# Performance work log

Measured on AMD Instinct MI355X. Metric: run time of the kernel, lower is better.

The kernel has to match this reference:

```python
import jax, jax.numpy as jnp
import numpy as np

# Dimensions (see shape_source)
U, B, D, H = 1024, 8, 512, 8
CHUNK = 32
NC = U // CHUNK          # 32 chunks
R, S, M = 32, 32, 32     # right-context rows, summary, memory
K = 31                   # depthwise conv kernel
Q = R + U + S            # 1088
KV = M + R + U           # 1088
NEG_INF = -1.0e8


def _build_attention_mask():
    """Chunk-wise Emformer mask: True = disallowed connection.
    Q layout: [R right-context rows | U utterance rows | S summary rows].
    KV layout: [M memory cols | R right-context cols | U utterance cols].
    Chunk c attends: memory banks < c, its own right-context col,
    its own chunk plus 1 left-context chunk of utterance."""
    mask = np.ones((Q, KV), dtype=bool)
    for c in range(NC):
        cols = np.zeros(KV, dtype=bool)
        cols[:min(c, M)] = True                    # memory of prior chunks
        cols[M + c] = True                         # this chunk's right context
        lo = max(0, c - 1) * CHUNK                 # 1 chunk of left context
        hi = (c + 1) * CHUNK
        cols[M + R + lo:M + R + hi] = True
        rows = [c] + list(range(R + c * CHUNK, R + (c + 1) * CHUNK)) + [R + U + c]
        mask[np.ix_(rows, np.nonzero(cols)[0])] = False
    return mask


def setup_inputs() -> dict:
    key = jax.random.key(0)
    ks = jax.random.split(key, 16)
    s = D ** -0.5
    inp = {
        'utterance': jax.random.normal(ks[0], (U, B, D), jnp.float32),
        'right_context': jax.random.normal(ks[1], (R, B, D), jnp.float32),
        'summary': jax.random.normal(ks[2], (S, B, D), jnp.float32),
        'memory': jax.random.normal(ks[3], (M, B, D), jnp.float32),
        'w_q': jax.random.normal(ks[4], (D, D), jnp.float32) * s,
        'b_q': jnp.zeros((D,), jnp.float32),
        'w_kv': jax.random.normal(ks[5], (2 * D, D), jnp.float32) * s,
        'b_kv': jnp.zeros((2 * D,), jnp.float32),
        'w_out': jax.random.normal(ks[6], (D, D), jnp.float32) * s,
        'b_out': jnp.zeros((D,), jnp.float32),
        'w_pw1': jax.random.normal(ks[7], (2 * D, D), jnp.float32) * s,
        'b_pw1': jnp.zeros((2 * D,), jnp.float32),
        'w_dw': jax.random.normal(ks[8], (D, 1, K), jnp.float32) * (K ** -0.5),
        'b_dw': jnp.zeros((D,), jnp.float32),
        'ln_g': jnp.ones((D,), jnp.float32),
        'ln_b': jnp.zeros((D,), jnp.float32),
        'w_pw2': jax.random.normal(ks[9], (D, D), jnp.float32) * s,
        'b_pw2': jnp.zeros((D,), jnp.float32),
        'lengths': jax.random.randint(ks[10], (B,), U // 2, U + 1, jnp.int32),
        'attention_mask': jnp.asarray(_build_attention_mask()),
    }
    return inp


def _conv_module(x, w_pw1, b_pw1, w_dw, b_dw, ln_g, ln_b, w_pw2, b_pw2):
    # x: (T, B, C) -> (B, C, T)
    x = x.transpose(1, 2, 0)
    x = jnp.einsum('bct,oc->bot', x, w_pw1) + b_pw1[:, None]
    a, g = jnp.split(x, 2, axis=1)
    x = a * jax.nn.sigmoid(g)                       # GLU over channel dim
    pad = (K - 1) // 2
    x = jax.lax.conv_general_dilated(
        x, w_dw, (1,), [(pad, pad)],
        dimension_numbers=('NCH', 'OIH', 'NCH'),
        feature_group_count=x.shape[1]) + b_dw[:, None]
    x = x.transpose(0, 2, 1)                        # (B, T, C) for LayerNorm
    mu = x.mean(-1, keepdims=True)
    var = ((x - mu) ** 2).mean(-1, keepdims=True)
    x = (x - mu) * jax.lax.rsqrt(var + 1e-5) * ln_g + ln_b
    x = x.transpose(0, 2, 1)
    x = x * jax.nn.sigmoid(x)                       # Swish
    x = jnp.einsum('bct,oc->bot', x, w_pw2) + b_pw2[:, None]
    return x.transpose(2, 0, 1)                     # (T, B, C)


def _emformer_forward(utterance, right_context, summary, memory,
                      w_q, b_q, w_kv, b_kv, w_out, b_out,
                      w_pw1, b_pw1, w_dw, b_dw, ln_g, ln_b, w_pw2, b_pw2,
                      lengths, attention_mask):
    d = D // H
    scaling = d ** -0.5
    q_in = jnp.concatenate([right_context, utterance, summary], axis=0)   # (Q,B,D)
    query = q_in @ w_q.T + b_q
    kv_in = jnp.concatenate([memory, right_context, utterance], axis=0)   # (KV,B,D)
    kv = kv_in @ w_kv.T + b_kv
    key_t, value_t = jnp.split(kv, 2, axis=2)

    def heads(t):  # (T,B,D) -> (B*H, T, d)
        return t.reshape(t.shape[0], B * H, d).transpose(1, 0, 2)

    qh, kh, vh = heads(query) * scaling, heads(key_t), heads(value_t)
    w = jnp.einsum('bqd,bkd->bqk', qh, kh)                                # (B*H,Q,KV)
    w = jnp.where(attention_mask[None], NEG_INF, w)
    # padding mask: pad positions are kv index >= KV - U + length
    pad = jnp.arange(KV)[None, :] >= (KV - U + lengths)[:, None]          # (B,KV)
    w = jnp.where(pad[:, None, :].repeat(H, axis=1).reshape(B * H, 1, KV), NEG_INF, w)
    p = jax.nn.softmax(w, axis=-1)
    attn = jnp.einsum('bqk,bkd->bqd', p, vh)                              # (B*H,Q,d)
    attn = attn.transpose(1, 0, 2).reshape(Q, B, D)
    outputs = attn @ w_out.T + b_out
    out_ru = outputs[:R + U]                                              # (R+U,B,D)
    # conformer convolution module with residual
    conv_out = _conv_module(out_ru, w_pw1, b_pw1, w_dw, b_dw,
                            ln_g, ln_b, w_pw2, b_pw2)
    return out_ru + conv_out


def reference(utterance, right_context, summary, memory,
              w_q, b_q, w_kv, b_kv, w_out, b_out,
              w_pw1, b_pw1, w_dw, b_dw, ln_g, ln_b, w_pw2, b_pw2,
              lengths, attention_mask):
    return _emformer_forward(utterance, right_context, summary, memory,
                             w_q, b_q, w_kv, b_kv, w_out, b_out,
                             w_pw1, b_pw1, w_dw, b_dw, ln_g, ln_b,
                             w_pw2, b_pw2, lengths, attention_mask)
```

## Files before the change

kernel.cpp:

```cpp
#include <hip/hip_runtime.h>
#include <hip/hip_bf16.h>
#include <math.h>

#define TQ    1056
#define TKV   1088

typedef __attribute__((ext_vector_type(8))) short short8;
typedef __attribute__((ext_vector_type(4))) short short4v;
typedef __attribute__((ext_vector_type(4))) float float4v;
typedef unsigned short ushort_t;

__device__ inline ushort_t f2bf(float x){
  union{float f; unsigned u;} v; v.f = x;
  unsigned r = v.u + 0x7fff + ((v.u >> 16) & 1);
  return (ushort_t)(r >> 16);
}
__device__ inline float bf2f(ushort_t h){
  union{unsigned u; float f;} v; v.u = ((unsigned)h) << 16;
  return v.f;
}

__device__ inline void gl_lds16(const ushort_t* g, ushort_t* l){
  __builtin_amdgcn_global_load_lds(
      (const __attribute__((address_space(1))) unsigned int*)g,
      (__attribute__((address_space(3))) unsigned int*)l, 16, 0, 0);
}

struct Cvt9 {
  const float* s[8];
  ushort_t*    d[8];
  const float* wdw;
  float*       wdwT;
  int bstart[9];
};

__global__ __launch_bounds__(256)
void cvt_f32_bf16(Cvt9 a)
{
  int blk = blockIdx.x;
  if (blk >= a.bstart[8]){
    int k = blk - a.bstart[8];
    int c = threadIdx.x;
    a.wdwT[k * 512 + c]       = a.wdw[c * 31 + k];
    a.wdwT[k * 512 + c + 256] = a.wdw[(c + 256) * 31 + k];
    return;
  }
  int seg = 0;
  while (blk >= a.bstart[seg + 1]) ++seg;
  int local = blk - a.bstart[seg];
  int idx = (local * 256 + threadIdx.x) * 4;
  float4v v = *(const float4v*)(a.s[seg] + idx);
  short4v o;
  #pragma unroll
  for (int j = 0; j < 4; ++j) ((ushort_t*)&o)[j] = f2bf(v[j]);
  *(short4v*)(a.d[seg] + idx) = o;
}

template<int MODE, int NX, int NT>
__global__ __launch_bounds__(256)
void gemm_bf16(const ushort_t* __restrict__ A, const ushort_t* __restrict__ Wb,
               const float* __restrict__ bias, const float* __restrict__ bias2,
               const ushort_t* __restrict__ residb,
               float* __restrict__ C0, ushort_t* __restrict__ U0,
               ushort_t* __restrict__ U1, ushort_t* __restrict__ Uv, int ny)
{
  constexpr int JN = NT / 32;
  const int blk = blockIdx.x;
  const int xcd = blk & 7;
  const int j   = blk >> 3;
  const int n_idx = j % NX;
  const int m_idx = (j / NX) * 8 + xcd;
  if (m_idx >= ny) return;

  __shared__ __align__(16) ushort_t As[128 * 64];
  __shared__ __align__(16) ushort_t Bs[NT * 64];
  const int tid  = threadIdx.x;
  const int w    = tid >> 6;
  const int lane = tid & 63;
  const int quad = lane >> 4;
  const int l16  = lane & 15;
  const int n0 = n_idx * NT;
  const int m0 = m_idx * 128;
  const int wm = (w >> 1) * 64;
  const int wn = (w & 1) * (NT / 2);
  const int srow = tid >> 3;
  const int skseg = tid & 7;

  float4v acc[4][JN];
  #pragma unroll
  for (int i = 0; i < 4; ++i)
    #pragma unroll
    for (int jj = 0; jj < JN; ++jj)
      acc[i][jj] = (float4v)(0.f);

  for (int kt = 0; kt < 8; ++kt){
    const int k0 = kt * 64;
    #pragma unroll
    for (int s = 0; s < 4; ++s){
      int row = s*32 + srow;
      gl_lds16(A + (size_t)(m0 + row) * 512 + k0 + ((skseg ^ (row & 7)) << 3),
               &As[row * 64 + (skseg << 3)]);
    }
    #pragma unroll
    for (int s = 0; s < NT/32; ++s){
      int row = s*32 + srow;
      gl_lds16(Wb + (size_t)(n0 + row) * 512 + k0 + ((skseg ^ (row & 7)) << 3),
               &Bs[row * 64 + (skseg << 3)]);
    }
    __syncthreads();
    #pragma unroll
    for (int kc = 0; kc < 2; ++kc){
      const int col = (((quad + (kc << 2)) ^ (l16 & 7)) << 3);
      short8 af[4], bf[JN];
      #pragma unroll
      for (int i = 0; i < 4; ++i)
        af[i] = *(const short8*)&As[(wm + i*16 + l16) * 64 + col];
      #pragma unroll
      for (int jj = 0; jj < JN; ++jj)
        bf[jj] = *(const short8*)&Bs[(wn + jj*16 + l16) * 64 + col];
      #pragma unroll
      for (int i = 0; i < 4; ++i)
        #pragma unroll
        for (int jj = 0; jj < JN; ++jj)
          acc[i][jj] = __builtin_amdgcn_mfma_f32_16x16x32_bf16(
                          af[i], bf[jj], acc[i][jj], 0, 0, 0);
    }
    __syncthreads();
  }

  #pragma unroll
  for (int jj = 0; jj < JN; ++jj){
    const int n = n0 + wn + jj*16 + l16;
    const float bn = (MODE == 4) ? (n < 512 ? bias[n] : bias2[(n - 512) & 1023])
                                 : bias[n];
    #pragma unroll
    for (int i = 0; i < 4; ++i){
      #pragma unroll
      for (int reg = 0; reg < 4; ++reg){
        const int m = m0 + wm + i*16 + quad*4 + reg;
        float v = acc[i][jj][reg] + bn;
        if (MODE == 4){
          int t = m >> 3, b = m & 7;
          if (n < 512){
            if (m >= 256){
              int mq = m - 256;
              int tq = mq >> 3, bq = mq & 7;
              int h = n >> 6, dh = n & 63;
              U0[(((size_t)(bq*8 + h)) * TQ + tq) * 64 + dh] = f2bf(v * 0.125f);
            }
          } else {
            int n2 = n & 511;
            int h = n2 >> 6, dh = n2 & 63;
            ushort_t* dst = (n < 1024) ? U1 : Uv;
            dst[(((size_t)(b*8 + h)) * TKV + t) * 64 + dh] = f2bf(v);
          }
        } else if (MODE == 0){
          U0[(size_t)m * 512 + n] = f2bf(v);
        } else {
          v += bf2f(residb[(size_t)m * 512 + n]);
          C0[(size_t)m * 512 + n] = v;
        }
      }
    }
  }
}

__global__ __launch_bounds__(256)
void transpose_v(const ushort_t* __restrict__ vh, ushort_t* __restrict__ vt)
{
  const int t0 = blockIdx.x * 64;
  const int bh = blockIdx.y;
  const int tid = threadIdx.x;
  __shared__ __align__(16) ushort_t T[64 * 72];

  #pragma unroll
  for (int e = 0; e < 2; ++e){
    int idx = e * 256 + tid;
    int r = idx >> 3, sg = (idx & 7) * 8;
    *(short8*)&T[r * 72 + sg] =
        *(const short8*)&vh[(((size_t)bh) * TKV + t0 + r) * 64 + sg];
  }
  __syncthreads();

  const int dh = tid & 63;
  const int ts = (tid >> 6) * 16;
  short8 v0, v1;
  #pragma unroll
  for (int j = 0; j < 8; ++j){
    ((ushort_t*)&v0)[j] = T[(ts + j) * 72 + dh];
    ((ushort_t*)&v1)[j] = T[(ts + 8 + j) * 72 + dh];
  }
  const size_t ob = (((size_t)bh) * 64 + dh) * TKV + t0 + ts;
  *(short8*)&vt[ob]     = v0;
  *(short8*)&vt[ob + 8] = v1;
}

#define PSTR 136

__global__ __launch_bounds__(256)
void attn_mfma(const ushort_t* __restrict__ qh, const ushort_t* __restrict__ kh,
               const ushort_t* __restrict__ vt, const int* __restrict__ lengths,
               ushort_t* __restrict__ attn_out)
{
  const int c  = blockIdx.x;
  const int bh = blockIdx.y;
  const int b  = bh >> 3, h = bh & 7;
  const int tid = threadIdx.x;
  const int w   = tid >> 6;
  const int lane = tid & 63;
  const int quad = lane >> 4;
  const int l16  = lane & 15;
  const int len  = lengths[b];
  const int tb2 = 64 + (c > 0 ? c - 1 : 0) * 32;
  const int tb3 = 64 + c * 32;

  __shared__ __align__(16) ushort_t Ps[48 * PSTR];

  const int basew = (w == 0) ? 0 : (w == 1) ? 32 : (w == 2) ? tb2 : tb3;

  float4v Sf[3][2];
  #pragma unroll
  for (int mt = 0; mt < 3; ++mt)
    #pragma unroll
    for (int jt = 0; jt < 2; ++jt)
      Sf[mt][jt] = (float4v)(0.f);

  #pragma unroll
  for (int kc = 0; kc < 2; ++kc){
    short8 bfr[2];
    #pragma unroll
    for (int jt = 0; jt < 2; ++jt)
      bfr[jt] = *(const short8*)&kh[((size_t)bh * TKV + basew + jt*16 + l16) * 64
                                    + kc*32 + quad*8];
    #pragma unroll
    for (int mt = 0; mt < 3; ++mt){
      int trow = (mt == 0) ? c : 32 + c*32 + (mt-1)*16 + l16;
      short8 afr = *(const short8*)&qh[((size_t)bh * TQ + trow) * 64
                                       + kc*32 + quad*8];
      if (mt == 0 && l16 != 0){
        short8 z = {0,0,0,0,0,0,0,0};
        afr = z;
      }
      #pragma unroll
      for (int jt = 0; jt < 2; ++jt)
        Sf[mt][jt] = __builtin_amdgcn_mfma_f32_16x16x32_bf16(
                        afr, bfr[jt], Sf[mt][jt], 0, 0, 0);
    }
  }

  bool live[2];
  #pragma unroll
  for (int jt = 0; jt < 2; ++jt){
    int jcol = jt*16 + l16;
    if      (w == 0) live[jt] = (jcol < c);
    else if (w == 1) live[jt] = (jcol == c);
    else if (w == 2) live[jt] = (c > 0) && ((c-1)*32 + jcol < len);
    else             live[jt] = (c*32 + jcol < len);
  }
  #pragma unroll
  for (int mt = 0; mt < 3; ++mt)
    #pragma unroll
    for (int jt = 0; jt < 2; ++jt)
      #pragma unroll
      for (int r = 0; r < 4; ++r){
        int row = mt*16 + quad*4 + r;
        Ps[row * PSTR + w*32 + jt*16 + l16] =
            live[jt] ? f2bf(__expf(Sf[mt][jt][r])) : (ushort_t)0;
      }
  __syncthreads();

  const short8 ones = {0x3F80,0x3F80,0x3F80,0x3F80,0x3F80,0x3F80,0x3F80,0x3F80};
  float4v Of[3], Ls[3];
  #pragma unroll
  for (int mt = 0; mt < 3; ++mt){ Of[mt] = (float4v)(0.f); Ls[mt] = (float4v)(0.f); }
  #pragma unroll
  for (int kc = 0; kc < 4; ++kc){
    const int tbase = (kc == 0) ? 0 : (kc == 1) ? 32 : (kc == 2) ? tb2 : tb3;
    short8 bv = *(const short8*)&vt[((size_t)bh * 64 + w*16 + l16) * TKV
                                    + tbase + quad*8];
    #pragma unroll
    for (int mt = 0; mt < 3; ++mt){
      short8 ap = *(const short8*)&Ps[(mt*16 + l16) * PSTR + kc*32 + quad*8];
      Of[mt] = __builtin_amdgcn_mfma_f32_16x16x32_bf16(ap, bv,   Of[mt], 0,0,0);
      Ls[mt] = __builtin_amdgcn_mfma_f32_16x16x32_bf16(ap, ones, Ls[mt], 0,0,0);
    }
  }

  #pragma unroll
  for (int mt = 0; mt < 3; ++mt){
    #pragma unroll
    for (int r = 0; r < 4; ++r){
      int row = mt*16 + quad*4 + r;
      if (mt == 0 && row != 0) continue;
      float o = Of[mt][r] / Ls[mt][r];
      int t = (mt == 0) ? c : 32 + c*32 + (row - 16);
      attn_out[(((size_t)t) * 8 + b) * 512 + h*64 + w*16 + l16] = f2bf(o);
    }
  }
}

__global__ __launch_bounds__(256)
void gemm_pw1_glu(const ushort_t* __restrict__ A, const ushort_t* __restrict__ Wb,
                  const float* __restrict__ bias, ushort_t* __restrict__ G, int ny)
{
  const int blk = blockIdx.x;
  const int xcd = blk & 7;
  const int j   = blk >> 3;
  const int n_idx = j % 8;
  const int m_idx = (j / 8) * 8 + xcd;
  if (m_idx >= ny) return;

  __shared__ __align__(16) ushort_t As [128 * 64];
  __shared__ __align__(16) ushort_t Bsa[64 * 64];
  __shared__ __align__(16) ushort_t Bsg[64 * 64];
  const int tid  = threadIdx.x;
  const int w    = tid >> 6;
  const int lane = tid & 63;
  const int quad = lane >> 4;
  const int l16  = lane & 15;
  const int n0 = n_idx * 64;
  const int m0 = m_idx * 128;
  const int wm = (w >> 1) * 64;
  const int wn = (w & 1) * 32;
  const int srow = tid >> 3;
  const int skseg = tid & 7;

  float4v acca[4][2], accg[4][2];
  #pragma unroll
  for (int i = 0; i < 4; ++i)
    #pragma unroll
    for (int jj = 0; jj < 2; ++jj){
      acca[i][jj] = (float4v)(0.f);
      accg[i][jj] = (float4v)(0.f);
    }

  for (int kt = 0; kt < 8; ++kt){
    const int k0 = kt * 64;
    #pragma unroll
    for (int s = 0; s < 4; ++s){
      int row = s*32 + srow;
      gl_lds16(A + (size_t)(m0 + row) * 512 + k0 + ((skseg ^ (row & 7)) << 3),
               &As[row * 64 + (skseg << 3)]);
    }
    #pragma unroll
    for (int s = 0; s < 2; ++s){
      int row = s*32 + srow;
      gl_lds16(Wb + (size_t)(n0 + row) * 512 + k0 + ((skseg ^ (row & 7)) << 3),
               &Bsa[row * 64 + (skseg << 3)]);
      gl_lds16(Wb + (size_t)(n0 + 512 + row) * 512 + k0 + ((skseg ^ (row & 7)) << 3),
               &Bsg[row * 64 + (skseg << 3)]);
    }
    __syncthreads();
    #pragma unroll
    for (int kc = 0; kc < 2; ++kc){
      const int col = (((quad + (kc << 2)) ^ (l16 & 7)) << 3);
      short8 af[4], ba[2], bg[2];
      #pragma unroll
      for (int i = 0; i < 4; ++i)
        af[i] = *(const short8*)&As[(wm + i*16 + l16) * 64 + col];
      #pragma unroll
      for (int jj = 0; jj < 2; ++jj){
        ba[jj] = *(const short8*)&Bsa[(wn + jj*16 + l16) * 64 + col];
        bg[jj] = *(const short8*)&Bsg[(wn + jj*16 + l16) * 64 + col];
      }
      #pragma unroll
      for (int i = 0; i < 4; ++i)
        #pragma unroll
        for (int jj = 0; jj < 2; ++jj){
          acca[i][jj] = __builtin_amdgcn_mfma_f32_16x16x32_bf16(
                           af[i], ba[jj], acca[i][jj], 0, 0, 0);
          accg[i][jj] = __builtin_amdgcn_mfma_f32_16x16x32_bf16(
                           af[i], bg[jj], accg[i][jj], 0, 0, 0);
        }
    }
    __syncthreads();
  }

  #pragma unroll
  for (int jj = 0; jj < 2; ++jj){
    const int n = n0 + wn + jj*16 + l16;
    const float bna = bias[n];
    const float bng = bias[n + 512];
    #pragma unroll
    for (int i = 0; i < 4; ++i){
      #pragma unroll
      for (int reg = 0; reg < 4; ++reg){
        const int m = m0 + wm + i*16 + quad*4 + reg;
        float a = acca[i][jj][reg] + bna;
        float g = accg[i][jj][reg] + bng;
        G[(size_t)m * 512 + n] = f2bf(a * (1.f / (1.f + __expf(-g))));
      }
    }
  }
}

__global__ __launch_bounds__(512)
void conv_ln_silu3(const ushort_t* __restrict__ glub,
                   const float* __restrict__ w_dwT, const float* __restrict__ b_dw,
                   const float* __restrict__ ln_g, const float* __restrict__ ln_b,
                   ushort_t* __restrict__ zb)
{
  const int b  = blockIdx.y;
  const int t0 = blockIdx.x * 16;
  const int tid = threadIdx.x;
  __shared__ __align__(16) char smem[47104];
  ushort_t* in_t = (ushort_t*)smem;
  float*    S    = (float*)smem;

  for (int e = tid; e < 2944; e += 512){
    int row = e >> 6, sg = (e & 63) * 8;
    int tt = t0 - 15 + row;
    short8 v = {0,0,0,0,0,0,0,0};
    if (tt >= 0 && tt < TQ)
      v = *(const short8*)&glub[((size_t)tt * 8 + b) * 512 + sg];
    *(short8*)&in_t[row * 512 + sg] = v;
  }
  float wreg[31];
  #pragma unroll
  for (int k = 0; k < 31; ++k) wreg[k] = w_dwT[k * 512 + tid];
  const float bd = b_dw[tid];
  __syncthreads();

  float col[46];
  #pragma unroll 2
  for (int rr = 0; rr < 46; ++rr) col[rr] = bf2f(in_t[rr * 512 + tid]);

  float r[16];
  #pragma unroll
  for (int t = 0; t < 16; ++t){
    float acc = bd;
    #pragma unroll
    for (int k = 0; k < 31; ++k) acc += col[t + k] * wreg[k];
    r[t] = acc;
  }
  __syncthreads();
  #pragma unroll
  for (int t = 0; t < 16; ++t) S[t * 512 + tid] = r[t];
  __syncthreads();

  const int tg = tid >> 5;
  const int l  = tid & 31;
  float s = 0.f;
  #pragma unroll
  for (int i = 0; i < 16; ++i) s += S[tg * 512 + l + 32*i];
  #pragma unroll
  for (int off = 16; off >= 1; off >>= 1) s += __shfl_xor(s, off);
  const float mu = s * (1.f / 512.f);
  float s2 = 0.f;
  #pragma unroll
  for (int i = 0; i < 16; ++i){
    float d = S[tg * 512 + l + 32*i] - mu;
    s2 += d * d;
  }
  #pragma unroll
  for (int off = 16; off >= 1; off >>= 1) s2 += __shfl_xor(s2, off);
  const float rs = rsqrtf(s2 * (1.f / 512.f) + 1e-5f);

  const int c0 = l * 16;
  ushort_t ov[16];
  #pragma unroll
  for (int e = 0; e < 4; ++e){
    float4v xv = *(const float4v*)&S[tg * 512 + c0 + e*4];
    float4v gv = *(const float4v*)&ln_g[c0 + e*4];
    float4v bv = *(const float4v*)&ln_b[c0 + e*4];
    #pragma unroll
    for (int jj = 0; jj < 4; ++jj){
      float xn = (xv[jj] - mu) * rs * gv[jj] + bv[jj];
      ov[e*4 + jj] = f2bf(xn * (1.f / (1.f + __expf(-xn))));
    }
  }
  const size_t obase = ((size_t)(t0 + tg) * 8 + b) * 512 + c0;
  *(short8*)&zb[obase]     = *(short8*)&ov[0];
  *(short8*)&zb[obase + 8] = *(short8*)&ov[8];
}

extern "C" void kernel_launch(void* const* d_in, const int* in_sizes, int n_in,
                              void* d_out, int out_size, void* d_ws, size_t ws_size,
                              hipStream_t stream)
{
  (void)in_sizes; (void)n_in; (void)out_size; (void)ws_size;
  const float* utter = (const float*)d_in[0];
  const float* rctx  = (const float*)d_in[1];
  const float* memry = (const float*)d_in[3];
  const float* b_q   = (const float*)d_in[5];
  const float* b_kv  = (const float*)d_in[7];
  const float* b_out = (const float*)d_in[9];
  const float* b_pw1 = (const float*)d_in[11];
  const float* w_dw  = (const float*)d_in[12];
  const float* b_dw  = (const float*)d_in[13];
  const float* ln_g  = (const float*)d_in[14];
  const float* ln_b  = (const float*)d_in[15];
  const float* b_pw2 = (const float*)d_in[17];
  const int* lengths = (const int*)d_in[18];

  ushort_t* u = (ushort_t*)d_ws;
  ushort_t* memB  = u;
  ushort_t* rcB   = memB  + 131072;
  ushort_t* uttB  = rcB   + 131072;
  ushort_t* wqB   = uttB  + 4194304;
  ushort_t* wkvB  = wqB   + 262144;
  ushort_t* woutB = wkvB  + 524288;
  ushort_t* wpw1B = woutB + 262144;
  ushort_t* wpw2B = wpw1B + 524288;
  ushort_t* q_h   = wpw2B + 262144;
  ushort_t* k_h   = q_h   + 4325376;
  ushort_t* v_h   = k_h   + 4456448;
  ushort_t* v_t   = v_h   + 4456448;
  ushort_t* attnb = v_t   + 4456448;
  ushort_t* outru_bf = attnb + 4325376;
  float*    wdwT  = (float*)(outru_bf + 4325376);
  ushort_t* glub  = q_h;
  ushort_t* zb    = attnb;
  float* outp = (float*)d_out;

  const ushort_t* A_kv = memB;

  Cvt9 ca;
  ca.s[0] = memry;                 ca.d[0] = memB;
  ca.s[1] = rctx;                  ca.d[1] = rcB;
  ca.s[2] = utter;                 ca.d[2] = uttB;
  ca.s[3] = (const float*)d_in[4]; ca.d[3] = wqB;
  ca.s[4] = (const float*)d_in[6]; ca.d[4] = wkvB;
  ca.s[5] = (const float*)d_in[8]; ca.d[5] = woutB;
  ca.s[6] = (const float*)d_in[10];ca.d[6] = wpw1B;
  ca.s[7] = (const float*)d_in[16];ca.d[7] = wpw2B;
  ca.wdw = w_dw; ca.wdwT = wdwT;
  int cnt[8] = {131072,131072,4194304,262144,524288,262144,524288,262144};
  int acc = 0;
  for (int i = 0; i < 8; ++i){ ca.bstart[i] = acc; acc += cnt[i] / 1024; }
  ca.bstart[8] = acc;
  cvt_f32_bf16<<<dim3(acc + 31), 256, 0, stream>>>(ca);

  gemm_bf16<4, 12, 128><<<dim3(8 * 9 * 12), 256, 0, stream>>>(
      A_kv, wqB, b_q, b_kv, nullptr, nullptr, q_h, k_h, v_h, 68);
  transpose_v<<<dim3(17, 64), 256, 0, stream>>>(v_h, v_t);
  attn_mfma<<<dim3(32, 64), 256, 0, stream>>>(q_h, k_h, v_t, lengths, attnb);
  gemm_bf16<0, 8, 64><<<dim3(8 * 9 * 8), 256, 0, stream>>>(
      attnb, woutB, b_out, nullptr, nullptr, nullptr, outru_bf, nullptr, nullptr, 66);
  gemm_pw1_glu<<<dim3(8 * 9 * 8), 256, 0, stream>>>(outru_bf, wpw1B, b_pw1, glub, 66);
  conv_ln_silu3<<<dim3(66, 8), 512, 0, stream>>>(glub, wdwT, b_dw, ln_g, ln_b, zb);
  gemm_bf16<3, 8, 64><<<dim3(8 * 9 * 8), 256, 0, stream>>>(
      zb, wpw2B, b_pw2, nullptr, outru_bf, outp, nullptr, nullptr, nullptr, 66);
}
```

Measured before the change: 254.1 us.

## Load GEMM operands straight from global into registers and restructure depthwise conv loop

The projection, output, and pointwise GEMMs stop staging A and B tiles in LDS through global_load_lds plus barriers. Each wave now loads its MFMA fragments directly from global memory into registers, dropping the LDS traffic and the synchronisation. The cost is that reuse across waves now depends on cache, and the loads are less coalesced 16-byte row-strided accesses. The depthwise conv is also reordered to stream each input row once and scatter it into 16 accumulators, which avoids holding a 46-element column in registers.

```diff
diff --git a/kernel.cpp b/kernel.cpp
--- a/kernel.cpp
+++ b/kernel.cpp
@@ -18,12 +18,6 @@
 __device__ inline float bf2f(ushort_t h){
   union{unsigned u; float f;} v; v.u = ((unsigned)h) << 16;
   return v.f;
-}
-
-__device__ inline void gl_lds16(const ushort_t* g, ushort_t* l){
-  __builtin_amdgcn_global_load_lds(
-      (const __attribute__((address_space(1))) unsigned int*)g,
-      (__attribute__((address_space(3))) unsigned int*)l, 16, 0, 0);
 }
 
 struct Cvt9 {
@@ -72,8 +66,6 @@
   const int m_idx = (j / NX) * 8 + xcd;
   if (m_idx >= ny) return;
 
-  __shared__ __align__(16) ushort_t As[128 * 64];
-  __shared__ __align__(16) ushort_t Bs[NT * 64];
   const int tid  = threadIdx.x;
   const int w    = tid >> 6;
   const int lane = tid & 63;
@@ -83,8 +75,6 @@
   const int m0 = m_idx * 128;
   const int wm = (w >> 1) * 64;
   const int wn = (w & 1) * (NT / 2);
-  const int srow = tid >> 3;
-  const int skseg = tid & 7;
 
   float4v acc[4][JN];
   #pragma unroll
@@ -93,39 +83,25 @@
     for (int jj = 0; jj < JN; ++jj)
       acc[i][jj] = (float4v)(0.f);
 
-  for (int kt = 0; kt < 8; ++kt){
-    const int k0 = kt * 64;
-    #pragma unroll
-    for (int s = 0; s < 4; ++s){
-      int row = s*32 + srow;
-      gl_lds16(A + (size_t)(m0 + row) * 512 + k0 + ((skseg ^ (row & 7)) << 3),
-               &As[row * 64 + (skseg << 3)]);
-    }
-    #pragma unroll
-    for (int s = 0; s < NT/32; ++s){
-      int row = s*32 + srow;
-      gl_lds16(Wb + (size_t)(n0 + row) * 512 + k0 + ((skseg ^ (row & 7)) << 3),
-               &Bs[row * 64 + (skseg << 3)]);
-    }
-    __syncthreads();
-    #pragma unroll
-    for (int kc = 0; kc < 2; ++kc){
-      const int col = (((quad + (kc << 2)) ^ (l16 & 7)) << 3);
-      short8 af[4], bf[JN];
-      #pragma unroll
-      for (int i = 0; i < 4; ++i)
-        af[i] = *(const short8*)&As[(wm + i*16 + l16) * 64 + col];
+  const ushort_t* Ab = A  + (size_t)(m0 + wm + l16) * 512 + quad * 8;
+  const ushort_t* Bb = Wb + (size_t)(n0 + wn + l16) * 512 + quad * 8;
+
+  #pragma unroll 2
+  for (int kt = 0; kt < 16; ++kt){
+    const int k0 = kt * 32;
+    short8 af[4], bf[JN];
+    #pragma unroll
+    for (int i = 0; i < 4; ++i)
+      af[i] = *(const short8*)(Ab + (size_t)(i*16) * 512 + k0);
+    #pragma unroll
+    for (int jj = 0; jj < JN; ++jj)
+      bf[jj] = *(const short8*)(Bb + (size_t)(jj*16) * 512 + k0);
+    #pragma unroll
+    for (int i = 0; i < 4; ++i)
       #pragma unroll
       for (int jj = 0; jj < JN; ++jj)
-        bf[jj] = *(const short8*)&Bs[(wn + jj*16 + l16) * 64 + col];
-      #pragma unroll
-      for (int i = 0; i < 4; ++i)
-        #pragma unroll
-        for (int jj = 0; jj < JN; ++jj)
-          acc[i][jj] = __builtin_amdgcn_mfma_f32_16x16x32_bf16(
-                          af[i], bf[jj], acc[i][jj], 0, 0, 0);
-    }
-    __syncthreads();
+        acc[i][jj] = __builtin_amdgcn_mfma_f32_16x16x32_bf16(
+                        af[i], bf[jj], acc[i][jj], 0, 0, 0);
   }
 
   #pragma unroll
@@ -166,6 +142,81 @@
 }
 
 __global__ __launch_bounds__(256)
+void gemm_pw1_glu(const ushort_t* __restrict__ A, const ushort_t* __restrict__ Wb,
+                  const float* __restrict__ bias, ushort_t* __restrict__ G, int ny)
+{
+  const int blk = blockIdx.x;
+  const int xcd = blk & 7;
+  const int j   = blk >> 3;
+  const int n_idx = j % 8;
+  const int m_idx = (j / 8) * 8 + xcd;
+  if (m_idx >= ny) return;
+
+  const int tid  = threadIdx.x;
+  const int w    = tid >> 6;
+  const int lane = tid & 63;
+  const int quad = lane >> 4;
+  const int l16  = lane & 15;
+  const int n0 = n_idx * 64;
+  const int m0 = m_idx * 128;
+  const int wm = (w >> 1) * 64;
+  const int wn = (w & 1) * 32;
+
+  float4v acca[4][2], accg[4][2];
+  #pragma unroll
+  for (int i = 0; i < 4; ++i)
+    #pragma unroll
+    for (int jj = 0; jj < 2; ++jj){
+      acca[i][jj] = (float4v)(0.f);
+      accg[i][jj] = (float4v)(0.f);
+    }
+
+  const ushort_t* Ab  = A  + (size_t)(m0 + wm + l16) * 512 + quad * 8;
+  const ushort_t* Bab = Wb + (size_t)(n0 + wn + l16) * 512 + quad * 8;
+  const ushort_t* Bgb = Bab + (size_t)512 * 512;
+
+  #pragma unroll 2
+  for (int kt = 0; kt < 16; ++kt){
+    const int k0 = kt * 32;
+    short8 af[4], ba[2], bg[2];
+    #pragma unroll
+    for (int i = 0; i < 4; ++i)
+      af[i] = *(const short8*)(Ab + (size_t)(i*16) * 512 + k0);
+    #pragma unroll
+    for (int jj = 0; jj < 2; ++jj){
+      ba[jj] = *(const short8*)(Bab + (size_t)(jj*16) * 512 + k0);
+      bg[jj] = *(const short8*)(Bgb + (size_t)(jj*16) * 512 + k0);
+    }
+    #pragma unroll
+    for (int i = 0; i < 4; ++i)
+      #pragma unroll
+      for (int jj = 0; jj < 2; ++jj){
+        acca[i][jj] = __builtin_amdgcn_mfma_f32_16x16x32_bf16(
+                         af[i], ba[jj], acca[i][jj], 0, 0, 0);
+        accg[i][jj] = __builtin_amdgcn_mfma_f32_16x16x32_bf16(
+                         af[i], bg[jj], accg[i][jj], 0, 0, 0);
+      }
+  }
+
+  #pragma unroll
+  for (int jj = 0; jj < 2; ++jj){
+    const int n = n0 + wn + jj*16 + l16;
+    const float bna = bias[n];
+    const float bng = bias[n + 512];
+    #pragma unroll
+    for (int i = 0; i < 4; ++i){
+      #pragma unroll
+      for (int reg = 0; reg < 4; ++reg){
+        const int m = m0 + wm + i*16 + quad*4 + reg;
+        float a = acca[i][jj][reg] + bna;
+        float g = accg[i][jj][reg] + bng;
+        G[(size_t)m * 512 + n] = f2bf(a * (1.f / (1.f + __expf(-g))));
+      }
+    }
+  }
+}
+
+__global__ __launch_bounds__(256)
 void transpose_v(const ushort_t* __restrict__ vh, ushort_t* __restrict__ vt)
 {
   const int t0 = blockIdx.x * 64;
@@ -299,103 +350,8 @@
   }
 }
 
-__global__ __launch_bounds__(256)
-void gemm_pw1_glu(const ushort_t* __restrict__ A, const ushort_t* __restrict__ Wb,
-                  const float* __restrict__ bias, ushort_t* __restrict__ G, int ny)
-{
-  const int blk = blockIdx.x;
-  const int xcd = blk & 7;
-  const int j   = blk >> 3;
-  const int n_idx = j % 8;
-  const int m_idx = (j / 8) * 8 + xcd;
-  if (m_idx >= ny) return;
-
-  __shared__ __align__(16) ushort_t As [128 * 64];
-  __shared__ __align__(16) ushort_t Bsa[64 * 64];
-  __shared__ __align__(16) ushort_t Bsg[64 * 64];
-  const int tid  = threadIdx.x;
-  const int w    = tid >> 6;
-  const int lane = tid & 63;
-  const int quad = lane >> 4;
-  const int l16  = lane & 15;
-  const int n0 = n_idx * 64;
-  const int m0 = m_idx * 128;
-  const int wm = (w >> 1) * 64;
-  const int wn = (w & 1) * 32;
-  const int srow = tid >> 3;
-  const int skseg = tid & 7;
-
-  float4v acca[4][2], accg[4][2];
-  #pragma unroll
-  for (int i = 0; i < 4; ++i)
-    #pragma unroll
-    for (int jj = 0; jj < 2; ++jj){
-      acca[i][jj] = (float4v)(0.f);
-      accg[i][jj] = (float4v)(0.f);
-    }
-
-  for (int kt = 0; kt < 8; ++kt){
-    const int k0 = kt * 64;
-    #pragma unroll
-    for (int s = 0; s < 4; ++s){
-      int row = s*32 + srow;
-      gl_lds16(A + (size_t)(m0 + row) * 512 + k0 + ((skseg ^ (row & 7)) << 3),
-               &As[row * 64 + (skseg << 3)]);
-    }
-    #pragma unroll
-    for (int s = 0; s < 2; ++s){
-      int row = s*32 + srow;
-      gl_lds16(Wb + (size_t)(n0 + row) * 512 + k0 + ((skseg ^ (row & 7)) << 3),
-               &Bsa[row * 64 + (skseg << 3)]);
-      gl_lds16(Wb + (size_t)(n0 + 512 + row) * 512 + k0 + ((skseg ^ (row & 7)) << 3),
-               &Bsg[row * 64 + (skseg << 3)]);
-    }
-    __syncthreads();
-    #pragma unroll
-    for (int kc = 0; kc < 2; ++kc){
-      const int col = (((quad + (kc << 2)) ^ (l16 & 7)) << 3);
-      short8 af[4], ba[2], bg[2];
-      #pragma unroll
-      for (int i = 0; i < 4; ++i)
-        af[i] = *(const short8*)&As[(wm + i*16 + l16) * 64 + col];
-      #pragma unroll
-      for (int jj = 0; jj < 2; ++jj){
-        ba[jj] = *(const short8*)&Bsa[(wn + jj*16 + l16) * 64 + col];
-        bg[jj] = *(const short8*)&Bsg[(wn + jj*16 + l16) * 64 + col];
-      }
-      #pragma unroll
-      for (int i = 0; i < 4; ++i)
-        #pragma unroll
-        for (int jj = 0; jj < 2; ++jj){
-          acca[i][jj] = __builtin_amdgcn_mfma_f32_16x16x32_bf16(
-                           af[i], ba[jj], acca[i][jj], 0, 0, 0);
-          accg[i][jj] = __builtin_amdgcn_mfma_f32_16x16x32_bf16(
-                           af[i], bg[jj], accg[i][jj], 0, 0, 0);
-        }
-    }
-    __syncthreads();
-  }
-
-  #pragma unroll
-  for (int jj = 0; jj < 2; ++jj){
-    const int n = n0 + wn + jj*16 + l16;
-    const float bna = bias[n];
-    const float bng = bias[n + 512];
-    #pragma unroll
-    for (int i = 0; i < 4; ++i){
-      #pragma unroll
-      for (int reg = 0; reg < 4; ++reg){
-        const int m = m0 + wm + i*16 + quad*4 + reg;
-        float a = acca[i][jj][reg] + bna;
-        float g = accg[i][jj][reg] + bng;
-        G[(size_t)m * 512 + n] = f2bf(a * (1.f / (1.f + __expf(-g))));
-      }
-    }
-  }
-}
-
 __global__ __launch_bounds__(512)
-void conv_ln_silu3(const ushort_t* __restrict__ glub,
+void conv_ln_silu4(const ushort_t* __restrict__ glub,
                    const float* __restrict__ w_dwT, const float* __restrict__ b_dw,
                    const float* __restrict__ ln_g, const float* __restrict__ ln_b,
                    ushort_t* __restrict__ zb)
@@ -421,17 +377,19 @@
   const float bd = b_dw[tid];
   __syncthreads();
 
-  float col[46];
-  #pragma unroll 2
-  for (int rr = 0; rr < 46; ++rr) col[rr] = bf2f(in_t[rr * 512 + tid]);
-
   float r[16];
   #pragma unroll
-  for (int t = 0; t < 16; ++t){
-    float acc = bd;
-    #pragma unroll
-    for (int k = 0; k < 31; ++k) acc += col[t + k] * wreg[k];
-    r[t] = acc;
+  for (int t = 0; t < 16; ++t) r[t] = bd;
+
+  #pragma unroll
+  for (int rr = 0; rr < 46; ++rr){
+    float v = bf2f(in_t[rr * 512 + tid]);
+    const int tlo = (rr > 30) ? rr - 30 : 0;
+    const int thi = (rr < 15) ? rr : 15;
+    #pragma unroll
+    for (int t = 0; t < 16; ++t)
+      if (t >= tlo && t <= thi)
+        r[t] += v * wreg[rr - t];
   }
   __syncthreads();
   #pragma unroll
@@ -538,7 +496,7 @@
   gemm_bf16<0, 8, 64><<<dim3(8 * 9 * 8), 256, 0, stream>>>(
       attnb, woutB, b_out, nullptr, nullptr, nullptr, outru_bf, nullptr, nullptr, 66);
   gemm_pw1_glu<<<dim3(8 * 9 * 8), 256, 0, stream>>>(outru_bf, wpw1B, b_pw1, glub, 66);
-  conv_ln_silu3<<<dim3(66, 8), 512, 0, stream>>>(glub, wdwT, b_dw, ln_g, ln_b, zb);
+  conv_ln_silu4<<<dim3(66, 8), 512, 0, stream>>>(glub, wdwT, b_dw, ln_g, ln_b, zb);
   gemm_bf16<3, 8, 64><<<dim3(8 * 9 * 8), 256, 0, stream>>>(
       zb, wpw2B, b_pw2, nullptr, outru_bf, outp, nullptr, nullptr, nullptr, 66);
 }
```

Result: slower. 347.7 us (+36.9%).
